# Kernel tuning notes

Hardware: AMD Instinct MI355X
Metric: run time of the kernel (lower is better)

The kernel has to match this reference:

```python
import jax, jax.numpy as jnp
import numpy as np

HEADS = 8


def setup_inputs() -> dict:
    key = jax.random.key(0)
    ks = jax.random.split(key, 6)
    B, N, D = 4, 2048, 512
    return {
        "x": jax.random.normal(ks[0], (B, N, D), dtype=jnp.float32),
        "pos": jax.random.uniform(ks[1], (B, N, 3), dtype=jnp.float32),
        "qkv_w": jax.random.normal(ks[2], (3 * D, D), dtype=jnp.float32) * 0.02,
        "qkv_b": jax.random.normal(ks[3], (3 * D,), dtype=jnp.float32) * 0.02,
        "out_w": jax.random.normal(ks[4], (D, D), dtype=jnp.float32) * 0.02,
        "out_b": jax.random.normal(ks[5], (D,), dtype=jnp.float32) * 0.02,
    }


def reference(x, pos, qkv_w, qkv_b, out_w, out_b):
    B, N, D = x.shape
    H = HEADS
    Dh = D // H
    scale = D ** (-0.5)  # NOTE: original uses full dim, not head dim

    # QKV projection -> [3, B, H, N, Dh]
    qkv = (x @ qkv_w.T + qkv_b).reshape(B, N, 3, H, Dh).transpose(2, 0, 3, 1, 4)
    q, k, v = qkv[0], qkv[1], qkv[2]

    # partial 3D RoPE on first 6 head dims (3 axis pairs)
    theta = pos * jnp.pi                    # [B, N, 3]
    sin = jnp.sin(theta)[:, None]           # [B, 1, N, 3] broadcasts over heads
    cos = jnp.cos(theta)[:, None]

    def rotate(t):
        x_rot = t[..., :6]
        x1 = x_rot[..., 0::2]               # [B, H, N, 3]
        x2 = x_rot[..., 1::2]
        return jnp.concatenate(
            [x1 * cos - x2 * sin, x1 * sin + x2 * cos, t[..., 6:]], axis=-1
        )

    q = rotate(q)
    k = rotate(k)

    attn = jax.nn.softmax(jnp.einsum("bhqd,bhkd->bhqk", q, k) * scale, axis=-1)
    out = jnp.einsum("bhqk,bhkd->bhqd", attn, v)          # [B, H, N, Dh]
    out = out.transpose(0, 2, 1, 3).reshape(B, N, D)
    return out @ out_w.T + out_b
```

## Files before the change

### kernel.cpp

```cpp
#include <hip/hip_runtime.h>
#include <stdint.h>

typedef __attribute__((ext_vector_type(4))) float f32x4;
typedef __attribute__((ext_vector_type(16))) float f32x16;
typedef __attribute__((ext_vector_type(8))) short bf16x8;
typedef __attribute__((ext_vector_type(4))) unsigned short u16x4;

__device__ __forceinline__ unsigned short f2bf(float f) {
    unsigned int u = __builtin_bit_cast(unsigned int, f);
    u += 0x7fffu + ((u >> 16) & 1u);
    return (unsigned short)(u >> 16);
}
__device__ __forceinline__ float bf2f(unsigned short s) {
    unsigned int u = ((unsigned int)s) << 16;
    return __builtin_bit_cast(float, u);
}
__device__ __forceinline__ float fexp2(float x) {
#if __has_builtin(__builtin_amdgcn_exp2f)
    return __builtin_amdgcn_exp2f(x);
#else
    return exp2f(x);
#endif
}
__device__ __forceinline__ unsigned int cvt_pk_bf16(float lo, float hi) {
    unsigned int r;
    asm("v_cvt_pk_bf16_f32 %0, %1, %2" : "=v"(r) : "v"(lo), "v"(hi));
    return r;
}

__global__ void k_cvt3(const float* __restrict__ x,
                       const float* __restrict__ w1,
                       const float* __restrict__ w2,
                       unsigned short* __restrict__ out) {
    const int C1 = 1048576;
    const int C2 = 196608;
    int i = blockIdx.x * blockDim.x + threadIdx.x;
    f32x4 v;
    if (i < C1)            v = ((const f32x4*)x)[i];
    else if (i < C1 + C2)  v = ((const f32x4*)w1)[i - C1];
    else                   v = ((const f32x4*)w2)[i - C1 - C2];
    u16x4 o;
    o.x = f2bf(v.x); o.y = f2bf(v.y); o.z = f2bf(v.z); o.w = f2bf(v.w);
    ((u16x4*)out)[i] = o;
}

template<int OUT_BF16>
__global__ __launch_bounds__(256, 2)
void k_gemm_nt(const unsigned short* __restrict__ A,
               const unsigned short* __restrict__ Bm,
               const float* __restrict__ bias,
               void* __restrict__ Cout, int M, int N, int K) {
    __shared__ unsigned short As[2][128 * 32];
    __shared__ unsigned short Bs[2][128 * 32];
    const int tid = threadIdx.x;
    const int lane = tid & 63;
    const int w = tid >> 6;
    const int wr = (w >> 1) * 64, wc = (w & 1) * 64;
    const int g = lane >> 4, fr = lane & 15;

    f32x4 acc[4][4];
#pragma unroll
    for (int i = 0; i < 4; ++i)
#pragma unroll
        for (int j = 0; j < 4; ++j) acc[i][j] = f32x4{0.f, 0.f, 0.f, 0.f};

    const int srow16 = lane >> 2;
    const int schunk = ((lane & 3) ^ (srow16 & 3)) * 8;
    const int sA = w, sB = w + 4;
    const unsigned short* Aseg0 = A + (size_t)(blockIdx.x * 128 + sA * 16 + srow16) * K + schunk;
    const unsigned short* Aseg1 = A + (size_t)(blockIdx.x * 128 + sB * 16 + srow16) * K + schunk;
    const unsigned short* Bseg0 = Bm + (size_t)(blockIdx.y * 128 + sA * 16 + srow16) * K + schunk;
    const unsigned short* Bseg1 = Bm + (size_t)(blockIdx.y * 128 + sB * 16 + srow16) * K + schunk;

    auto stage = [&](int bsel, int k0) {
        char* la = (char*)&As[bsel][0];
        char* lb = (char*)&Bs[bsel][0];
        __builtin_amdgcn_global_load_lds((const __attribute__((address_space(1))) void*)(Aseg0 + k0),
                                         (__attribute__((address_space(3))) void*)(la + sA * 1024), 16, 0, 0);
        __builtin_amdgcn_global_load_lds((const __attribute__((address_space(1))) void*)(Aseg1 + k0),
                                         (__attribute__((address_space(3))) void*)(la + sB * 1024), 16, 0, 0);
        __builtin_amdgcn_global_load_lds((const __attribute__((address_space(1))) void*)(Bseg0 + k0),
                                         (__attribute__((address_space(3))) void*)(lb + sA * 1024), 16, 0, 0);
        __builtin_amdgcn_global_load_lds((const __attribute__((address_space(1))) void*)(Bseg1 + k0),
                                         (__attribute__((address_space(3))) void*)(lb + sB * 1024), 16, 0, 0);
    };
    auto compute = [&](int bsel) {
        bf16x8 af[4], bfv[4];
        const int rc = (g ^ (fr & 3)) * 8;
#pragma unroll
        for (int mi = 0; mi < 4; ++mi)
            af[mi] = *(const bf16x8*)&As[bsel][(wr + mi * 16 + fr) * 32 + rc];
#pragma unroll
        for (int ni = 0; ni < 4; ++ni)
            bfv[ni] = *(const bf16x8*)&Bs[bsel][(wc + ni * 16 + fr) * 32 + rc];
        __builtin_amdgcn_s_setprio(1);
#pragma unroll
        for (int mi = 0; mi < 4; ++mi)
#pragma unroll
            for (int ni = 0; ni < 4; ++ni)
                acc[mi][ni] = __builtin_amdgcn_mfma_f32_16x16x32_bf16(af[mi], bfv[ni], acc[mi][ni], 0, 0, 0);
        __builtin_amdgcn_s_setprio(0);
    };

    const int nt = K >> 5;
    stage(0, 0);
    asm volatile("s_waitcnt vmcnt(0)" ::: "memory");
    __builtin_amdgcn_s_barrier();
    int cur = 0;
#pragma unroll 1
    for (int t = 0; t < nt; ++t) {
        if (t < nt - 1) stage(cur ^ 1, (t + 1) << 5);
        compute(cur);
        if (t < nt - 1) {
            asm volatile("s_waitcnt vmcnt(0)" ::: "memory");
            __builtin_amdgcn_s_barrier();
        }
        cur ^= 1;
    }

#pragma unroll
    for (int mi = 0; mi < 4; ++mi) {
#pragma unroll
        for (int ni = 0; ni < 4; ++ni) {
            int row = blockIdx.x * 128 + wr + mi * 16 + g * 4;
            int col = blockIdx.y * 128 + wc + ni * 16 + fr;
            float bz = bias[col];
#pragma unroll
            for (int r = 0; r < 4; ++r) {
                float v = acc[mi][ni][r] + bz;
                if (OUT_BF16) ((unsigned short*)Cout)[(size_t)(row + r) * N + col] = f2bf(v);
                else          ((float*)Cout)[(size_t)(row + r) * N + col] = v;
            }
        }
    }
}

__global__ void k_rotary(const unsigned short* __restrict__ qkv,
                         const float* __restrict__ pos,
                         unsigned short* __restrict__ Qb,
                         unsigned short* __restrict__ Kb,
                         unsigned short* __restrict__ VT) {
    const float PI = 3.14159265358979323846f;
    const float QS = 0.04419417382415922f * 1.44269504088896341f;
    int cid = blockIdx.x * 256 + threadIdx.x;
    int s = cid >> 19;
    int r = cid & 524287;
    if (s < 2) {
        int m = r >> 6, c = r & 63;
        int h = c >> 3, dc = c & 7;
        int b = m >> 11, n = m & 2047;
        bf16x8 v = *(const bf16x8*)&qkv[m * 1536 + s * 512 + c * 8];
        float f[8];
#pragma unroll
        for (int i = 0; i < 8; ++i) f[i] = bf2f((unsigned short)v[i]);
        if (dc == 0) {
            float nf[6];
#pragma unroll
            for (int j = 0; j < 3; ++j) {
                float th = pos[m * 3 + j] * PI;
                float sn = __sinf(th), cs = __cosf(th);
                float x1 = f[2 * j], x2 = f[2 * j + 1];
                nf[j] = x1 * cs - x2 * sn;
                nf[3 + j] = x1 * sn + x2 * cs;
            }
#pragma unroll
            for (int j = 0; j < 6; ++j) f[j] = nf[j];
        }
        if (s == 0) {
#pragma unroll
            for (int i = 0; i < 8; ++i) f[i] *= QS;
        }
        bf16x8 o;
#pragma unroll
        for (int i = 0; i < 8; ++i) o[i] = (short)f2bf(f[i]);
        unsigned short* dst = (s == 0) ? Qb : Kb;
        *(bf16x8*)&dst[((size_t)(b * 8 + h) * 2048 + n) * 64 + dc * 8] = o;
    } else {
        int cd = r >> 13;
        int m = r & 8191;
        int b = m >> 11, n = m & 2047;
        int h = cd >> 3, d8 = (cd & 7) * 8;
        bf16x8 v = *(const bf16x8*)&qkv[m * 1536 + 1024 + cd * 8];
        int q2 = (n >> 2) & 3;
        int np = n + (q2 == 1 ? 4 : (q2 == 2 ? -4 : 0));
        size_t base = ((size_t)(b * 8 + h) * 64 + d8) * 2048 + np;
#pragma unroll
        for (int i = 0; i < 8; ++i) VT[base + (size_t)i * 2048] = (unsigned short)v[i];
    }
}

__global__ __launch_bounds__(512, 4)
void k_attn(const unsigned short* __restrict__ Qb,
            const unsigned short* __restrict__ Kb,
            const unsigned short* __restrict__ VT,
            unsigned short* __restrict__ Ob) {
    __shared__ unsigned short smem[2][2][2][4096];
    const int tid = threadIdx.x, lane = tid & 63, w = tid >> 6;
    const int wl = w & 3, half = w >> 2;
    const int l31 = lane & 31, hi = lane >> 5;
    const int bid = blockIdx.x;
    const int bh = (bid & 7) * 4 + ((bid >> 3) >> 4);
    const int qb = (bid >> 3) & 15;
    const int b = bh >> 3, h = bh & 7;
    const int qr0 = qb * 128 + wl * 32;
    const unsigned short* Q = Qb + (size_t)bh * 2048 * 64;
    const unsigned short* K = Kb + (size_t)bh * 2048 * 64;
    const unsigned short* V = VT + (size_t)bh * 64 * 2048;
    const int thalf = half * 16;

    const int srow8 = lane >> 3;
    const int swc = ((lane & 7) ^ srow8) << 3;
    const int sA = wl, sB = wl + 4;

    bf16x8 bq[4];
#pragma unroll
    for (int ds = 0; ds < 4; ++ds)
        bq[ds] = *(const bf16x8*)&Q[(size_t)(qr0 + l31) * 64 + ds * 16 + hi * 8];

    f32x16 oT0, oT1;
#pragma unroll
    for (int i = 0; i < 16; ++i) { oT0[i] = 0.f; oT1[i] = 0.f; }
    float lpart = 0.f;

    auto stage = [&](int bsel, int t) {
        const int kv0 = t * 64;
        const unsigned short* k0 = K + (size_t)(kv0 + sA * 8 + srow8) * 64 + swc;
        const unsigned short* k1 = K + (size_t)(kv0 + sB * 8 + srow8) * 64 + swc;
        const unsigned short* v0 = V + (size_t)(sA * 8 + srow8) * 2048 + kv0 + swc;
        const unsigned short* v1 = V + (size_t)(sB * 8 + srow8) * 2048 + kv0 + swc;
        char* dk = (char*)&smem[half][0][bsel][0];
        char* dv = (char*)&smem[half][1][bsel][0];
        __builtin_amdgcn_global_load_lds((const __attribute__((address_space(1))) void*)k0,
                                         (__attribute__((address_space(3))) void*)(dk + sA * 1024), 16, 0, 0);
        __builtin_amdgcn_global_load_lds((const __attribute__((address_space(1))) void*)k1,
                                         (__attribute__((address_space(3))) void*)(dk + sB * 1024), 16, 0, 0);
        __builtin_amdgcn_global_load_lds((const __attribute__((address_space(1))) void*)v0,
                                         (__attribute__((address_space(3))) void*)(dv + sA * 1024), 16, 0, 0);
        __builtin_amdgcn_global_load_lds((const __attribute__((address_space(1))) void*)v1,
                                         (__attribute__((address_space(3))) void*)(dv + sB * 1024), 16, 0, 0);
    };

    auto pack8 = [&](const float* p) -> bf16x8 {
        union { unsigned int u[4]; bf16x8 v; } c;
        c.u[0] = cvt_pk_bf16(p[0], p[1]);
        c.u[1] = cvt_pk_bf16(p[2], p[3]);
        c.u[2] = cvt_pk_bf16(p[4], p[5]);
        c.u[3] = cvt_pk_bf16(p[6], p[7]);
        return c.v;
    };

    auto compute = [&](int bsel) {
        const unsigned short* KsC = &smem[half][0][bsel][0];
        const unsigned short* VtC = &smem[half][1][bsel][0];
        f32x16 s0, s1;
#pragma unroll
        for (int i = 0; i < 16; ++i) { s0[i] = 0.f; s1[i] = 0.f; }
        __builtin_amdgcn_s_setprio(1);
#pragma unroll
        for (int ds = 0; ds < 4; ++ds) {
            const int c = ((((ds << 1) | hi) ^ (l31 & 7)) << 3);
            bf16x8 ka0 = *(const bf16x8*)&KsC[l31 * 64 + c];
            bf16x8 ka1 = *(const bf16x8*)&KsC[(32 + l31) * 64 + c];
            s0 = __builtin_amdgcn_mfma_f32_32x32x16_bf16(ka0, bq[ds], s0, 0, 0, 0);
            s1 = __builtin_amdgcn_mfma_f32_32x32x16_bf16(ka1, bq[ds], s1, 0, 0, 0);
        }
        __builtin_amdgcn_s_setprio(0);
        float p0[16], p1[16];
        float lsum = 0.f;
#pragma unroll
        for (int r = 0; r < 16; ++r) {
            p0[r] = fexp2(s0[r]);
            p1[r] = fexp2(s1[r]);
            lsum += p0[r] + p1[r];
        }
        lpart += lsum;
        bf16x8 pb0 = pack8(p0);
        bf16x8 pb1 = pack8(p0 + 8);
        bf16x8 pb2 = pack8(p1);
        bf16x8 pb3 = pack8(p1 + 8);
        __builtin_amdgcn_s_setprio(1);
#pragma unroll
        for (int kb = 0; kb < 4; ++kb) {
            const int c = ((((kb << 1) | hi) ^ (l31 & 7)) << 3);
            bf16x8 av0 = *(const bf16x8*)&VtC[l31 * 64 + c];
            bf16x8 av1 = *(const bf16x8*)&VtC[(32 + l31) * 64 + c];
            bf16x8 pbk = (kb == 0) ? pb0 : (kb == 1) ? pb1 : (kb == 2) ? pb2 : pb3;
            oT0 = __builtin_amdgcn_mfma_f32_32x32x16_bf16(av0, pbk, oT0, 0, 0, 0);
            oT1 = __builtin_amdgcn_mfma_f32_32x32x16_bf16(av1, pbk, oT1, 0, 0, 0);
        }
        __builtin_amdgcn_s_setprio(0);
    };

    stage(0, thalf);
    asm volatile("s_waitcnt vmcnt(0)" ::: "memory");
    __builtin_amdgcn_s_barrier();
    int cur = 0;
#pragma unroll 1
    for (int t = 0; t < 16; ++t) {
        if (t < 15) stage(cur ^ 1, thalf + t + 1);
        compute(cur);
        if (t < 15) {
            asm volatile("s_waitcnt vmcnt(0)" ::: "memory");
            __builtin_amdgcn_s_barrier();
        }
        cur ^= 1;
    }

    __syncthreads();
    float* mrg = (float*)&smem[0][0][0][0];
    float* slot = mrg + (size_t)(wl * 64 + lane) * 33;
    if (half) {
#pragma unroll
        for (int i = 0; i < 16; ++i) { slot[i] = oT0[i]; slot[16 + i] = oT1[i]; }
        slot[32] = lpart;
    }
    __syncthreads();
    if (!half) {
#pragma unroll
        for (int i = 0; i < 16; ++i) { oT0[i] += slot[i]; oT1[i] += slot[16 + i]; }
        float lf = lpart + slot[32];
        lf += __shfl_xor(lf, 32, 64);
        float il = 1.f / lf;
        size_t rowbase = (size_t)(b * 2048 + qr0 + l31) * 512 + h * 64;
#pragma unroll
        for (int grp = 0; grp < 4; ++grp) {
            u16x4 o0, o1;
#pragma unroll
            for (int i = 0; i < 4; ++i) {
                o0[i] = f2bf(oT0[grp * 4 + i] * il);
                o1[i] = f2bf(oT1[grp * 4 + i] * il);
            }
            int dv0 = grp * 8 + 4 * hi;
            *(u16x4*)&Ob[rowbase + dv0] = o0;
            *(u16x4*)&Ob[rowbase + 32 + dv0] = o1;
        }
    }
}

extern "C" void kernel_launch(void* const* d_in, const int* in_sizes, int n_in,
                              void* d_out, int out_size, void* d_ws, size_t ws_size,
                              hipStream_t stream) {
    const float* x     = (const float*)d_in[0];
    const float* pos   = (const float*)d_in[1];
    const float* qkv_w = (const float*)d_in[2];
    const float* qkv_b = (const float*)d_in[3];
    const float* out_w = (const float*)d_in[4];
    const float* out_b = (const float*)d_in[5];
    float* out = (float*)d_out;

    unsigned short* Xb   = (unsigned short*)d_ws;
    unsigned short* W1b  = Xb   + (size_t)8192 * 512;
    unsigned short* W2b  = W1b  + (size_t)1536 * 512;
    unsigned short* QKVb = W2b  + (size_t)512 * 512;
    unsigned short* Qb   = QKVb + (size_t)8192 * 1536;
    unsigned short* Kb   = Qb   + (size_t)4194304;
    unsigned short* VTb  = Kb   + (size_t)4194304;
    unsigned short* Ob   = VTb  + (size_t)4194304;

    k_cvt3<<<5120, 256, 0, stream>>>(x, qkv_w, out_w, Xb);
    k_gemm_nt<1><<<dim3(64, 12), 256, 0, stream>>>(Xb, W1b, qkv_b, QKVb, 8192, 1536, 512);
    k_rotary<<<6144, 256, 0, stream>>>(QKVb, pos, Qb, Kb, VTb);
    k_attn<<<512, 512, 0, stream>>>(Qb, Kb, VTb, Ob);
    k_gemm_nt<0><<<dim3(64, 4), 256, 0, stream>>>(Ob, W2b, out_b, out, 8192, 512, 512);
}
```

Baseline: 94.75 us.

## Triple-buffer GEMM LDS staging and remap blocks for XCD-aware locality

The NT GEMM moves from double to triple buffering in LDS. The next-next tile is issued after compute, and the wait is relaxed to vmcnt(4), so one stage of loads stays in flight across each barrier. The 2D grid becomes a 1D launch with a block remap that gives each XCD a contiguous group of 8 row blocks, to improve L2 reuse of the A rows. Launch bounds rise to 3 blocks per SM and LDS use grows by half, which may change register allocation.

```diff
diff --git a/kernel.cpp b/kernel.cpp
--- a/kernel.cpp
+++ b/kernel.cpp
@@ -45,19 +45,25 @@
 }
 
 template<int OUT_BF16>
-__global__ __launch_bounds__(256, 2)
+__global__ __launch_bounds__(256, 3)
 void k_gemm_nt(const unsigned short* __restrict__ A,
                const unsigned short* __restrict__ Bm,
                const float* __restrict__ bias,
-               void* __restrict__ Cout, int M, int N, int K) {
-    __shared__ unsigned short As[2][128 * 32];
-    __shared__ unsigned short Bs[2][128 * 32];
+               void* __restrict__ Cout, int M, int N, int K, int colblocks) {
+    __shared__ unsigned short As[3][128 * 32];
+    __shared__ unsigned short Bs[3][128 * 32];
     const int tid = threadIdx.x;
     const int lane = tid & 63;
     const int w = tid >> 6;
     const int wr = (w >> 1) * 64, wc = (w & 1) * 64;
     const int g = lane >> 4, fr = lane & 15;
 
+    const int bid = blockIdx.x;
+    const int xcd = bid & 7, loc = bid >> 3;
+    const int rowb = xcd * 8 + (loc & 7);
+    const int colb = loc >> 3;
+    (void)colblocks;
+
     f32x4 acc[4][4];
 #pragma unroll
     for (int i = 0; i < 4; ++i)
@@ -67,10 +73,10 @@
     const int srow16 = lane >> 2;
     const int schunk = ((lane & 3) ^ (srow16 & 3)) * 8;
     const int sA = w, sB = w + 4;
-    const unsigned short* Aseg0 = A + (size_t)(blockIdx.x * 128 + sA * 16 + srow16) * K + schunk;
-    const unsigned short* Aseg1 = A + (size_t)(blockIdx.x * 128 + sB * 16 + srow16) * K + schunk;
-    const unsigned short* Bseg0 = Bm + (size_t)(blockIdx.y * 128 + sA * 16 + srow16) * K + schunk;
-    const unsigned short* Bseg1 = Bm + (size_t)(blockIdx.y * 128 + sB * 16 + srow16) * K + schunk;
+    const unsigned short* Aseg0 = A + (size_t)(rowb * 128 + sA * 16 + srow16) * K + schunk;
+    const unsigned short* Aseg1 = A + (size_t)(rowb * 128 + sB * 16 + srow16) * K + schunk;
+    const unsigned short* Bseg0 = Bm + (size_t)(colb * 128 + sA * 16 + srow16) * K + schunk;
+    const unsigned short* Bseg1 = Bm + (size_t)(colb * 128 + sB * 16 + srow16) * K + schunk;
 
     auto stage = [&](int bsel, int k0) {
         char* la = (char*)&As[bsel][0];
@@ -104,26 +110,27 @@
 
     const int nt = K >> 5;
     stage(0, 0);
-    asm volatile("s_waitcnt vmcnt(0)" ::: "memory");
-    __builtin_amdgcn_s_barrier();
+    stage(1, 32);
     int cur = 0;
 #pragma unroll 1
     for (int t = 0; t < nt; ++t) {
-        if (t < nt - 1) stage(cur ^ 1, (t + 1) << 5);
+        if (t < nt - 1) asm volatile("s_waitcnt vmcnt(4)" ::: "memory");
+        else            asm volatile("s_waitcnt vmcnt(0)" ::: "memory");
+        __builtin_amdgcn_s_barrier();
         compute(cur);
-        if (t < nt - 1) {
-            asm volatile("s_waitcnt vmcnt(0)" ::: "memory");
-            __builtin_amdgcn_s_barrier();
-        }
-        cur ^= 1;
+        if (t + 2 < nt) {
+            int nxt = cur + 2; if (nxt >= 3) nxt -= 3;
+            stage(nxt, (t + 2) << 5);
+        }
+        cur = (cur + 1 == 3) ? 0 : cur + 1;
     }
 
 #pragma unroll
     for (int mi = 0; mi < 4; ++mi) {
 #pragma unroll
         for (int ni = 0; ni < 4; ++ni) {
-            int row = blockIdx.x * 128 + wr + mi * 16 + g * 4;
-            int col = blockIdx.y * 128 + wc + ni * 16 + fr;
+            int row = rowb * 128 + wr + mi * 16 + g * 4;
+            int col = colb * 128 + wc + ni * 16 + fr;
             float bz = bias[col];
 #pragma unroll
             for (int r = 0; r < 4; ++r) {
@@ -358,8 +365,8 @@
     unsigned short* Ob   = VTb  + (size_t)4194304;
 
     k_cvt3<<<5120, 256, 0, stream>>>(x, qkv_w, out_w, Xb);
-    k_gemm_nt<1><<<dim3(64, 12), 256, 0, stream>>>(Xb, W1b, qkv_b, QKVb, 8192, 1536, 512);
+    k_gemm_nt<1><<<768, 256, 0, stream>>>(Xb, W1b, qkv_b, QKVb, 8192, 1536, 512, 12);
     k_rotary<<<6144, 256, 0, stream>>>(QKVb, pos, Qb, Kb, VTb);
     k_attn<<<512, 512, 0, stream>>>(Qb, Kb, VTb, Ob);
-    k_gemm_nt<0><<<dim3(64, 4), 256, 0, stream>>>(Ob, W2b, out_b, out, 8192, 512, 512);
-}
+    k_gemm_nt<0><<<256, 256, 0, stream>>>(Ob, W2b, out_b, out, 8192, 512, 512, 4);
+}
```

Result: no change. 93.34 us (-1.5%).
